# Kernel optimization log

Hardware: AMD Instinct MI355X
Metric: run time of the kernel (lower is better)

## Reference

```python
import jax, jax.numpy as jnp
import numpy as np

IN_FEATURES = 4096
OUT_FEATURES = 16384

def setup_inputs() -> dict:
    key = jax.random.key(0)
    k1, k2 = jax.random.split(key)
    x = jax.random.normal(k1, (4, 2048, IN_FEATURES), dtype=jnp.float32)
    # init_weights: uniform(-1, 1)
    W = jax.random.uniform(k2, (OUT_FEATURES, IN_FEATURES), dtype=jnp.float32, minval=-1.0, maxval=1.0)
    b = jnp.zeros((OUT_FEATURES,), dtype=jnp.float32)
    return {"x": x, "W": W, "b": b}

def reference(x, W, b):
    # Binarize weights to {-1, 0, +1} via sign, then dense linear: y = x @ sign(W)^T + b
    Wb = jnp.sign(W)
    return jnp.einsum('bsd,od->bso', x, Wb) + b
```

## Files before the change

### kernel.cpp

```cpp
#include <hip/hip_runtime.h>
#include <hip/hip_bf16.h>

#define M_TOT 8192
#define N_TOT 16384
#define K_TOT 4096
#define NT (K_TOT / 64)

typedef int i32x4 __attribute__((ext_vector_type(4)));
typedef int i32x16 __attribute__((ext_vector_type(16)));
typedef __bf16 bf16x8 __attribute__((ext_vector_type(8)));
typedef float f32x4 __attribute__((ext_vector_type(4)));

#define GLOAD_LDS16(g, l)                                                     \
  __builtin_amdgcn_global_load_lds(                                           \
      (__attribute__((address_space(1))) const void*)(g),                     \
      (__attribute__((address_space(3))) void*)(l), 16, 0, 0)

__device__ __forceinline__ ushort f2bf_rne(float f) {
  unsigned u = __float_as_uint(f);
  u += 0x7FFFu + ((u >> 16) & 1u);
  return (ushort)(u >> 16);
}
__device__ __forceinline__ ushort sgn_bf16(float w) {
  return w > 0.f ? (ushort)0x3F80u : (w < 0.f ? (ushort)0xBF80u : (ushort)0u);
}


__global__ void quant_x_kernel(const float* __restrict__ x,
                               char* __restrict__ At, float* __restrict__ s) {
  int row = blockIdx.x;
  int tid = threadIdx.x;
  const float4* xr = (const float4*)(x + (size_t)row * K_TOT + tid * 16);
  float4 v[4];
  float amax = 0.f;
#pragma unroll
  for (int j = 0; j < 4; ++j) {
    v[j] = xr[j];
    amax = fmaxf(amax, fmaxf(fmaxf(fabsf(v[j].x), fabsf(v[j].y)),
                             fmaxf(fabsf(v[j].z), fabsf(v[j].w))));
  }
#pragma unroll
  for (int o = 32; o > 0; o >>= 1) amax = fmaxf(amax, __shfl_xor(amax, o));
  __shared__ float wmax[4];
  if ((tid & 63) == 0) wmax[tid >> 6] = amax;
  __syncthreads();
  amax = fmaxf(fmaxf(wmax[0], wmax[1]), fmaxf(wmax[2], wmax[3]));
  float inv = amax > 0.f ? 127.0f / amax : 0.f;
  if (tid == 0) s[row] = amax * (1.0f / 127.0f);
  int q[16];
#pragma unroll
  for (int j = 0; j < 4; ++j) {
    q[j * 4 + 0] = max(-127, min(127, __float2int_rn(v[j].x * inv)));
    q[j * 4 + 1] = max(-127, min(127, __float2int_rn(v[j].y * inv)));
    q[j * 4 + 2] = max(-127, min(127, __float2int_rn(v[j].z * inv)));
    q[j * 4 + 3] = max(-127, min(127, __float2int_rn(v[j].w * inv)));
  }
  int4 o4;
  int* op = (int*)&o4;
#pragma unroll
  for (int j = 0; j < 4; ++j)
    op[j] = (q[j * 4] & 255) | ((q[j * 4 + 1] & 255) << 8) |
            ((q[j * 4 + 2] & 255) << 16) | ((q[j * 4 + 3] & 255) << 24);
  int r32 = row >> 5, l31 = row & 31;
  int kt = tid >> 2, ks = (tid >> 1) & 1, hi = tid & 1;
  size_t dst = ((size_t)(r32 * 128 + kt * 2 + ks) << 10) + ((hi * 32 + l31) << 4);
  *(int4*)(At + dst) = o4;
}

__global__ void quant_w_kernel(const float* __restrict__ w,
                               char* __restrict__ Bt) {
  int n32 = blockIdx.x;
  int t = threadIdx.x;
#pragma unroll 4
  for (int i = 0; i < 32; ++i) {
    int c = i * 256 + t;
    int kt = c >> 7, ks = (c >> 6) & 1, l = c & 63;
    int n = n32 * 32 + (l & 31);
    int k = kt * 64 + ks * 32 + (l >> 5) * 16;
    const float4* src = (const float4*)(w + (size_t)n * K_TOT + k);
    int4 o4;
    int* op = (int*)&o4;
#pragma unroll
    for (int j = 0; j < 4; ++j) {
      float4 v = src[j];
      int q0 = v.x > 0.f ? 1 : (v.x < 0.f ? -1 : 0);
      int q1 = v.y > 0.f ? 1 : (v.y < 0.f ? -1 : 0);
      int q2 = v.z > 0.f ? 1 : (v.z < 0.f ? -1 : 0);
      int q3 = v.w > 0.f ? 1 : (v.w < 0.f ? -1 : 0);
      op[j] = (q0 & 255) | ((q1 & 255) << 8) | ((q2 & 255) << 16) |
              ((q3 & 255) << 24);
    }
    *(int4*)(Bt + ((size_t)n32 << 17) + ((size_t)c << 4)) = o4;
  }
}

__global__ __launch_bounds__(256, 2) void gemm_i8_hyb(
    const char* __restrict__ At, const char* __restrict__ Bt,
    const float* __restrict__ s, const float* __restrict__ bias,
    float* __restrict__ C) {
  __shared__ char lds[4][16384];

  int bid = blockIdx.x;
  int wg = (bid & 7) * 512 + (bid >> 3);
  int bnS = wg >> 9;
  int rem = wg & 511;
  int bm = rem >> 4;
  int bn = bnS * 16 + (rem & 15);
  int rowBase = bm * 256;
  int colBase = bn * 128;

  int t = threadIdx.x;
  int lane = t & 63;
  int wave = t >> 6;
  int wr = wave >> 1;
  int wc = wave & 1;
  int l31 = lane & 31;
  int hi = lane >> 5;

  const char* gAp[4];
#pragma unroll
  for (int q = 0; q < 4; ++q) {
    int ss = t + 256 * q;
    int g = ss >> 6;
    int ks = g >> 3, rg = g & 7;
    gAp[q] = At + ((size_t)((bm * 8 + rg) * 128 + ks) << 10) + ((ss & 63) << 4);
  }
  const char* gBp[2];
#pragma unroll
  for (int ni = 0; ni < 2; ++ni)
    gBp[ni] = Bt + ((size_t)(bn * 4 + wc * 2 + ni) << 17) + (lane << 4);

  i32x16 acc[4][2] = {};
  i32x4 brA[2][2], brB[2][2];

#define STAGE_A(kt_, buf_)                                                    \
  {                                                                           \
    size_t _o = (size_t)(kt_) << 11;                                          \
    GLOAD_LDS16(gAp[0] + _o, &lds[buf_][t * 16]);                             \
    GLOAD_LDS16(gAp[1] + _o, &lds[buf_][4096 + t * 16]);                      \
    GLOAD_LDS16(gAp[2] + _o, &lds[buf_][8192 + t * 16]);                      \
    GLOAD_LDS16(gAp[3] + _o, &lds[buf_][12288 + t * 16]);                     \
  }
#define LOADB(kt_, dst)                                                       \
  {                                                                           \
    size_t _o = (size_t)(kt_) << 11;                                          \
    dst[0][0] = *(const i32x4*)(gBp[0] + _o);                                 \
    dst[0][1] = *(const i32x4*)(gBp[1] + _o);                                 \
    dst[1][0] = *(const i32x4*)(gBp[0] + _o + 1024);                          \
    dst[1][1] = *(const i32x4*)(gBp[1] + _o + 1024);                          \
  }
#define COMPUTE(buf_, bset)                                                   \
  {                                                                           \
    const char* _la = &lds[buf_][0];                                          \
    _Pragma("unroll") for (int ks = 0; ks < 2; ++ks) {                        \
      _Pragma("unroll") for (int mi = 0; mi < 4; ++mi) {                      \
        i32x4 _af = *(const i32x4*)(_la + ((ks * 8 + wr * 4 + mi) << 10) +    \
                                    (lane << 4));                             \
        acc[mi][0] = __builtin_amdgcn_mfma_i32_32x32x32_i8(                   \
            _af, bset[ks][0], acc[mi][0], 0, 0, 0);                           \
        acc[mi][1] = __builtin_amdgcn_mfma_i32_32x32x32_i8(                   \
            _af, bset[ks][1], acc[mi][1], 0, 0, 0);                           \
      }                                                                       \
    }                                                                         \
  }
#define TILE(kt_, buf_, bcur, bnxt)                                           \
  {                                                                           \
    STAGE_A((kt_) + 2, ((buf_) + 2) & 3);                                     \
    __builtin_amdgcn_sched_barrier(0);   \
    LOADB((kt_) + 1, bnxt);                                                   \
    COMPUTE(buf_, bcur);                                                      \
    __builtin_amdgcn_s_barrier();                                             \
    __builtin_amdgcn_sched_barrier(0);     \
  }

  STAGE_A(0, 0);
  STAGE_A(1, 1);
  LOADB(0, brA);
  asm volatile("s_waitcnt vmcnt(0)" ::: "memory");
  __builtin_amdgcn_s_barrier();
  __builtin_amdgcn_sched_barrier(0);

  for (int it = 0; it < 15; ++it) {
    int kt = it * 4;
    TILE(kt + 0, 0, brA, brB);
    TILE(kt + 1, 1, brB, brA);
    TILE(kt + 2, 2, brA, brB);
    TILE(kt + 3, 3, brB, brA);
  }
  {
    STAGE_A(62, 2);
    __builtin_amdgcn_sched_barrier(0);
    LOADB(61, brB);
    COMPUTE(0, brA);
    __builtin_amdgcn_s_barrier();
    __builtin_amdgcn_sched_barrier(0);

    STAGE_A(63, 3);
    __builtin_amdgcn_sched_barrier(0);
    LOADB(62, brA);
    COMPUTE(1, brB);
    __builtin_amdgcn_s_barrier();
    __builtin_amdgcn_sched_barrier(0);

    LOADB(63, brB);
    COMPUTE(2, brA);
    __builtin_amdgcn_s_barrier();
    __builtin_amdgcn_sched_barrier(0);

    COMPUTE(3, brB);
  }

#undef TILE
#undef COMPUTE
#undef LOADB
#undef STAGE_A

#pragma unroll
  for (int mi = 0; mi < 4; ++mi) {
#pragma unroll
    for (int ni = 0; ni < 2; ++ni) {
      int gc = colBase + wc * 64 + ni * 32 + l31;
      float bv = bias[gc];
#pragma unroll
      for (int rg = 0; rg < 16; ++rg) {
        int rowIn = (rg & 3) + 8 * (rg >> 2) + 4 * hi;
        int gr = rowBase + wr * 128 + mi * 32 + rowIn;
        C[(size_t)gr * N_TOT + gc] = (float)acc[mi][ni][rg] * s[gr] + bv;
      }
    }
  }
}

__global__ void gemm_fused_kernel(const float* __restrict__ A,
                                  const float* __restrict__ W,
                                  const float* __restrict__ bias,
                                  float* __restrict__ C) {
  __shared__ ushort lsA[128 * 32];
  __shared__ ushort lsB[128 * 32];

  int nwg = gridDim.x;
  int bid = blockIdx.x;
  int wg = (bid & 7) * (nwg >> 3) + (bid >> 3);
  const int NBN = N_TOT / 128;
  int bm = wg / NBN;
  int bn = wg % NBN;
  int rowBase = bm * 128;
  int colBase = bn * 128;

  int t = threadIdx.x;
  int lane = t & 63;
  int wave = t >> 6;
  int wm = (wave >> 1) * 64;
  int wn = (wave & 1) * 64;

  f32x4 acc[4][4] = {};

  int srow = t >> 3;
  int scol = (t & 7) * 4;
  int fr = lane & 15;
  int koff = (lane >> 4) * 8;

  for (int k0 = 0; k0 < K_TOT; k0 += 32) {
    float4 va[4], vb[4];
#pragma unroll
    for (int r = 0; r < 4; ++r) {
      va[r] = *(const float4*)&A[(size_t)(rowBase + r * 32 + srow) * K_TOT + k0 + scol];
      vb[r] = *(const float4*)&W[(size_t)(colBase + r * 32 + srow) * K_TOT + k0 + scol];
    }
    __syncthreads();
#pragma unroll
    for (int r = 0; r < 4; ++r) {
      int e = r * 1024 + t * 4;
      ushort4 oa, ob;
      oa.x = f2bf_rne(va[r].x); oa.y = f2bf_rne(va[r].y);
      oa.z = f2bf_rne(va[r].z); oa.w = f2bf_rne(va[r].w);
      ob.x = sgn_bf16(vb[r].x); ob.y = sgn_bf16(vb[r].y);
      ob.z = sgn_bf16(vb[r].z); ob.w = sgn_bf16(vb[r].w);
      *(ushort4*)&lsA[e] = oa;
      *(ushort4*)&lsB[e] = ob;
    }
    __syncthreads();

    bf16x8 af[4], bfr[4];
#pragma unroll
    for (int i = 0; i < 4; ++i)
      af[i] = *(const bf16x8*)&lsA[(wm + i * 16 + fr) * 32 + koff];
#pragma unroll
    for (int j = 0; j < 4; ++j)
      bfr[j] = *(const bf16x8*)&lsB[(wn + j * 16 + fr) * 32 + koff];

#pragma unroll
    for (int i = 0; i < 4; ++i)
#pragma unroll
      for (int j = 0; j < 4; ++j)
        acc[i][j] = __builtin_amdgcn_mfma_f32_16x16x32_bf16(af[i], bfr[j],
                                                            acc[i][j], 0, 0, 0);
  }

  int orow0 = rowBase + wm + ((lane >> 4) << 2);
  int ocol0 = colBase + wn + (lane & 15);
#pragma unroll
  for (int i = 0; i < 4; ++i) {
#pragma unroll
    for (int j = 0; j < 4; ++j) {
      int col = ocol0 + j * 16;
      float bv = bias[col];
#pragma unroll
      for (int rg = 0; rg < 4; ++rg) {
        int row = orow0 + i * 16 + rg;
        C[(size_t)row * N_TOT + col] = acc[i][j][rg] + bv;
      }
    }
  }
}

extern "C" void kernel_launch(void* const* d_in, const int* in_sizes, int n_in,
                              void* d_out, int out_size, void* d_ws,
                              size_t ws_size, hipStream_t stream) {
  const float* x = (const float*)d_in[0];
  const float* W = (const float*)d_in[1];
  const float* b = (const float*)d_in[2];
  float* out = (float*)d_out;

  const size_t xq_bytes = (size_t)M_TOT * K_TOT;
  const size_t wq_bytes = (size_t)N_TOT * K_TOT;
  const size_t need = xq_bytes + wq_bytes + M_TOT * 4;

  if (ws_size >= need) {
    char* At = (char*)d_ws;
    char* Bt = At + xq_bytes;
    float* s = (float*)(Bt + wq_bytes);
    quant_x_kernel<<<M_TOT, 256, 0, stream>>>(x, At, s);
    quant_w_kernel<<<N_TOT / 32, 256, 0, stream>>>(W, Bt);
    gemm_i8_hyb<<<4096, 256, 0, stream>>>(At, Bt, s, b, out);
  } else {
    const int nblocks = (M_TOT / 128) * (N_TOT / 128);
    gemm_fused_kernel<<<nblocks, 256, 0, stream>>>(x, W, b, out);
  }
}
```

Baseline: 782.6 us.

## Enlarge int8 GEMM tile to 256x256 with both operands staged via LDS

Replaces the 256x128 int8 MFMA GEMM (256 threads, B fragments loaded straight from global into registers) with a 256x256 tile run by 512 threads. Both A and B now go through a 4-deep LDS ring using direct global-to-LDS loads, with a counted vmcnt wait. The goal is to cut global traffic per MFMA through more reuse and to simplify the pipelined loop. In exchange, LDS use per block rises to 128KB, which limits residency to one block per CU, and the grid becomes smaller.

Result: faster. 679.9 us (-13.1%).

```diff
diff --git a/kernel.cpp b/kernel.cpp
--- a/kernel.cpp
+++ b/kernel.cpp
@@ -94,126 +94,94 @@
   }
 }
 
-__global__ __launch_bounds__(256, 2) void gemm_i8_hyb(
+__global__ __launch_bounds__(512, 2) void gemm_i8_big4(
     const char* __restrict__ At, const char* __restrict__ Bt,
     const float* __restrict__ s, const float* __restrict__ bias,
     float* __restrict__ C) {
-  __shared__ char lds[4][16384];
+  __shared__ char lds[4][32768];
 
   int bid = blockIdx.x;
-  int wg = (bid & 7) * 512 + (bid >> 3);
-  int bnS = wg >> 9;
-  int rem = wg & 511;
-  int bm = rem >> 4;
-  int bn = bnS * 16 + (rem & 15);
+  int wg = (bid & 7) * 256 + (bid >> 3);
+  int bnS = wg >> 8;
+  int rem = wg & 255;
+  int bm = rem >> 3;
+  int bn = bnS * 8 + (rem & 7);
   int rowBase = bm * 256;
-  int colBase = bn * 128;
+  int colBase = bn * 256;
 
   int t = threadIdx.x;
   int lane = t & 63;
   int wave = t >> 6;
-  int wr = wave >> 1;
-  int wc = wave & 1;
+  int wr = wave >> 2;
+  int wc = wave & 3;
   int l31 = lane & 31;
   int hi = lane >> 5;
 
-  const char* gAp[4];
-#pragma unroll
-  for (int q = 0; q < 4; ++q) {
-    int ss = t + 256 * q;
+  const char* gAp[2];
+  const char* gBp[2];
+#pragma unroll
+  for (int q = 0; q < 2; ++q) {
+    int ss = t + 512 * q;
     int g = ss >> 6;
-    int ks = g >> 3, rg = g & 7;
-    gAp[q] = At + ((size_t)((bm * 8 + rg) * 128 + ks) << 10) + ((ss & 63) << 4);
-  }
-  const char* gBp[2];
-#pragma unroll
-  for (int ni = 0; ni < 2; ++ni)
-    gBp[ni] = Bt + ((size_t)(bn * 4 + wc * 2 + ni) << 17) + (lane << 4);
+    int r32l = g >> 1, ks = g & 1;
+    int j = ss & 63;
+    gAp[q] = At + ((size_t)((bm * 8 + r32l) * 128 + ks) << 10) + (j << 4);
+    gBp[q] = Bt + ((size_t)((bn * 8 + r32l) * 128 + ks) << 10) + (j << 4);
+  }
 
   i32x16 acc[4][2] = {};
-  i32x4 brA[2][2], brB[2][2];
-
-#define STAGE_A(kt_, buf_)                                                    \
+
+#define STAGE(kt_, buf_)                                                      \
   {                                                                           \
     size_t _o = (size_t)(kt_) << 11;                                          \
     GLOAD_LDS16(gAp[0] + _o, &lds[buf_][t * 16]);                             \
-    GLOAD_LDS16(gAp[1] + _o, &lds[buf_][4096 + t * 16]);                      \
-    GLOAD_LDS16(gAp[2] + _o, &lds[buf_][8192 + t * 16]);                      \
-    GLOAD_LDS16(gAp[3] + _o, &lds[buf_][12288 + t * 16]);                     \
-  }
-#define LOADB(kt_, dst)                                                       \
-  {                                                                           \
-    size_t _o = (size_t)(kt_) << 11;                                          \
-    dst[0][0] = *(const i32x4*)(gBp[0] + _o);                                 \
-    dst[0][1] = *(const i32x4*)(gBp[1] + _o);                                 \
-    dst[1][0] = *(const i32x4*)(gBp[0] + _o + 1024);                          \
-    dst[1][1] = *(const i32x4*)(gBp[1] + _o + 1024);                          \
-  }
-#define COMPUTE(buf_, bset)                                                   \
+    GLOAD_LDS16(gAp[1] + _o, &lds[buf_][8192 + t * 16]);                      \
+    GLOAD_LDS16(gBp[0] + _o, &lds[buf_][16384 + t * 16]);                     \
+    GLOAD_LDS16(gBp[1] + _o, &lds[buf_][24576 + t * 16]);                     \
+  }
+#define COMPUTE(buf_)                                                         \
   {                                                                           \
     const char* _la = &lds[buf_][0];                                          \
+    const char* _lb = _la + 16384;                                            \
     _Pragma("unroll") for (int ks = 0; ks < 2; ++ks) {                        \
+      i32x4 bf0 = *(const i32x4*)(_lb + (((wc * 2 + 0) * 2 + ks) << 10) +     \
+                                  (lane << 4));                               \
+      i32x4 bf1 = *(const i32x4*)(_lb + (((wc * 2 + 1) * 2 + ks) << 10) +     \
+                                  (lane << 4));                               \
       _Pragma("unroll") for (int mi = 0; mi < 4; ++mi) {                      \
-        i32x4 _af = *(const i32x4*)(_la + ((ks * 8 + wr * 4 + mi) << 10) +    \
+        i32x4 _af = *(const i32x4*)(_la + (((wr * 4 + mi) * 2 + ks) << 10) +  \
                                     (lane << 4));                             \
         acc[mi][0] = __builtin_amdgcn_mfma_i32_32x32x32_i8(                   \
-            _af, bset[ks][0], acc[mi][0], 0, 0, 0);                           \
+            _af, bf0, acc[mi][0], 0, 0, 0);                                   \
         acc[mi][1] = __builtin_amdgcn_mfma_i32_32x32x32_i8(                   \
-            _af, bset[ks][1], acc[mi][1], 0, 0, 0);                           \
+            _af, bf1, acc[mi][1], 0, 0, 0);                                   \
       }                                                                       \
     }                                                                         \
   }
-#define TILE(kt_, buf_, bcur, bnxt)                                           \
-  {                                                                           \
-    STAGE_A((kt_) + 2, ((buf_) + 2) & 3);                                     \
-    __builtin_amdgcn_sched_barrier(0);   \
-    LOADB((kt_) + 1, bnxt);                                                   \
-    COMPUTE(buf_, bcur);                                                      \
-    __builtin_amdgcn_s_barrier();                                             \
-    __builtin_amdgcn_sched_barrier(0);     \
-  }
-
-  STAGE_A(0, 0);
-  STAGE_A(1, 1);
-  LOADB(0, brA);
-  asm volatile("s_waitcnt vmcnt(0)" ::: "memory");
+
+  STAGE(0, 0);
+  STAGE(1, 1);
+  asm volatile("s_waitcnt vmcnt(4)" ::: "memory");
+  __builtin_amdgcn_sched_barrier(0);
   __builtin_amdgcn_s_barrier();
   __builtin_amdgcn_sched_barrier(0);
 
-  for (int it = 0; it < 15; ++it) {
-    int kt = it * 4;
-    TILE(kt + 0, 0, brA, brB);
-    TILE(kt + 1, 1, brB, brA);
-    TILE(kt + 2, 2, brA, brB);
-    TILE(kt + 3, 3, brB, brA);
-  }
-  {
-    STAGE_A(62, 2);
+  for (int tt = 0; tt < NT; ++tt) {
+    int buf = tt & 3;
+    if (tt + 2 < NT) {
+      STAGE(tt + 2, (tt + 2) & 3);
+      asm volatile("s_waitcnt vmcnt(4)" ::: "memory");
+    } else if (tt + 1 < NT) {
+      asm volatile("s_waitcnt vmcnt(0)" ::: "memory");
+    }
+    COMPUTE(buf);
     __builtin_amdgcn_sched_barrier(0);
-    LOADB(61, brB);
-    COMPUTE(0, brA);
     __builtin_amdgcn_s_barrier();
     __builtin_amdgcn_sched_barrier(0);
-
-    STAGE_A(63, 3);
-    __builtin_amdgcn_sched_barrier(0);
-    LOADB(62, brA);
-    COMPUTE(1, brB);
-    __builtin_amdgcn_s_barrier();
-    __builtin_amdgcn_sched_barrier(0);
-
-    LOADB(63, brB);
-    COMPUTE(2, brA);
-    __builtin_amdgcn_s_barrier();
-    __builtin_amdgcn_sched_barrier(0);
-
-    COMPUTE(3, brB);
-  }
-
-#undef TILE
+  }
+
 #undef COMPUTE
-#undef LOADB
-#undef STAGE_A
+#undef STAGE
 
 #pragma unroll
   for (int mi = 0; mi < 4; ++mi) {
@@ -332,7 +300,8 @@
     float* s = (float*)(Bt + wq_bytes);
     quant_x_kernel<<<M_TOT, 256, 0, stream>>>(x, At, s);
     quant_w_kernel<<<N_TOT / 32, 256, 0, stream>>>(W, Bt);
-    gemm_i8_hyb<<<4096, 256, 0, stream>>>(At, Bt, s, b, out);
+    const int nblocks = (M_TOT / 256) * (N_TOT / 256);
+    gemm_i8_big4<<<nblocks, 512, 0, stream>>>(At, Bt, s, b, out);
   } else {
     const int nblocks = (M_TOT / 128) * (N_TOT / 128);
     gemm_fused_kernel<<<nblocks, 256, 0, stream>>>(x, W, b, out);
```
